# Kernel optimization log

Measured on AMD Instinct MI355X. Metric: run time of the kernel, lower is better.

The kernel has to match this reference:

```python
import jax, jax.numpy as jnp
import numpy as np

EPSILON = 0.1   # entropic regularization (reg)
TOL = 0.01      # stopThr
N_ITERS = 50    # numItermax
S_MASS = 0.9    # partial transported mass m (a,b normalized to sum 1 so s <= 1 is valid)
N, M = 2048, 2048


def _epot(C, a, b):
    """Faithful jax port of POT's entropic_partial_wasserstein with the EPOT
    module's marginal normalization. Fixed-point iteration with row-scaling,
    col-scaling, total-mass scaling and q1/q2/q3 correction matrices, with
    early-stop semantics (err checked every 10 iters) emulated via a done flag."""
    a = a / jnp.sum(a)
    b = b / jnp.sum(b)
    K0 = jnp.exp(-C / EPSILON)
    K0 = K0 * (S_MASS / jnp.sum(K0))
    ones = jnp.ones_like(K0)

    def body(carry, _):
        K, q1, q2, q3, err, cpt, done = carry
        Kprev = K
        # row scaling (clamped at 1 for partial mass)
        Kq = K * q1
        row = jnp.minimum(a / jnp.sum(Kq, axis=1), 1.0)          # (n,)
        K1 = row[:, None] * Kq
        q1n = q1 * Kprev / K1
        # col scaling
        K1prev = K1
        K1q = K1 * q2
        col = jnp.minimum(b / jnp.sum(K1q, axis=0), 1.0)         # (m,)
        K2 = K1q * col[None, :]
        q2n = q2 * K1prev / K2
        # total mass scaling
        K2prev = K2
        K2q = K2 * q3
        Kn = K2q * (S_MASS / jnp.sum(K2q))
        q3n = q3 * K2prev / Kn
        # POT updates err only every 10 iterations
        errn = jnp.where(cpt % 10 == 0,
                         jnp.sqrt(jnp.sum((Kprev - Kn) ** 2)), err)
        keep = lambda new, old: jnp.where(done, old, new)
        K = keep(Kn, K)
        q1 = keep(q1n, q1)
        q2 = keep(q2n, q2)
        q3 = keep(q3n, q3)
        err = jnp.where(done, err, errn)
        cpt = jnp.where(done, cpt, cpt + 1)
        done = done | (err <= TOL)
        return (K, q1, q2, q3, err, cpt, done), None

    init = (K0, ones, ones, ones, jnp.float32(1.0), jnp.int32(0),
            jnp.array(False))
    (K, _, _, _, _, _, _), _ = jax.lax.scan(body, init, None, length=N_ITERS)
    return K


def setup_inputs() -> dict:
    key = jax.random.key(0)
    k1, k2, k3 = jax.random.split(key, 3)
    C = jax.random.uniform(k1, (N, M), dtype=jnp.float32)
    a = jax.random.uniform(k2, (N,), dtype=jnp.float32) + 0.1
    b = jax.random.uniform(k3, (M,), dtype=jnp.float32) + 0.1
    return {"C": C, "a": a, "b": b}


def reference(C, a, b):
    return _epot(C, a, b)
```

## Files before the change

kernel.cpp:

```cpp
#include <hip/hip_runtime.h>

static constexpr int    N      = 2048;
static constexpr int    NBLK   = 256;
static constexpr int    NTHR   = 1024;
static constexpr int    RPB    = 8;
static constexpr double D_MASS = 0.9;
static constexpr double D_TOL  = 0.01;
static constexpr int    NITER  = 50;

struct Ws {
    double a_sum, b_sum;
    double bandSum[NBLK];
    double rowSum[N];
    double dotParts[NBLK];
    double errParts[NBLK];
    float  U[N], V[N];
    double Ud[N], rpD[N], Vd[N], cpD[N], UpD[N], VpD[N];
    float  partialT[(size_t)N * NBLK];
};

__device__ __forceinline__ double block_reduce(double v, double* s16) {
    for (int off = 32; off; off >>= 1) v += __shfl_xor(v, off, 64);
    const int wave = threadIdx.x >> 6, lane = threadIdx.x & 63;
    __syncthreads();
    if (lane == 0) s16[wave] = v;
    __syncthreads();
    double s = 0.0;
    #pragma unroll
    for (int w = 0; w < 16; ++w) s += s16[w];
    return s;
}

__global__ void __launch_bounds__(NTHR)
k1_sums(const float* __restrict__ C, const float* __restrict__ a,
        const float* __restrict__ b, Ws* __restrict__ ws)
{
    __shared__ double s16[16];
    const int tid = threadIdx.x, bid = blockIdx.x, lane = tid & 63;
    const int r0 = bid * RPB, rloc = tid >> 7, cgrp = tid & 127;

    if (bid == 0) {
        double t = block_reduce((double)a[tid] + (double)a[tid + 1024], s16);
        if (tid == 0) ws->a_sum = t;
    } else if (bid == 1) {
        double t = block_reduce((double)b[tid] + (double)b[tid + 1024], s16);
        if (tid == 0) ws->b_sum = t;
    }

    const int i = r0 + rloc;
    const float4* c4 = (const float4*)(C + (size_t)i * N);
    double s = 0.0;
    #pragma unroll 4
    for (int j4 = cgrp; j4 < N / 4; j4 += 128) {
        float4 c = c4[j4];
        s += (double)expf(-10.0f * c.x) + (double)expf(-10.0f * c.y)
           + (double)expf(-10.0f * c.z) + (double)expf(-10.0f * c.w);
    }
    for (int off = 32; off; off >>= 1) s += __shfl_xor(s, off, 64);
    __syncthreads();
    if (lane == 0) s16[tid >> 6] = s;
    __syncthreads();
    if (tid < RPB) ws->rowSum[r0 + tid] = s16[2 * tid] + s16[2 * tid + 1];
    if (tid == 0) {
        double bs = 0.0;
        #pragma unroll
        for (int w = 0; w < 16; ++w) bs += s16[w];
        ws->bandSum[bid] = bs;
    }
}

__global__ void __launch_bounds__(NTHR)
k2_rowscale_colpart(const float* __restrict__ C, const float* __restrict__ a,
                    Ws* __restrict__ ws)
{
    __shared__ double s16[16];
    __shared__ double sU[RPB];
    const int tid = threadIdx.x, bid = blockIdx.x;
    const int r0 = bid * RPB;

    const double k0sum = block_reduce((tid < NBLK) ? ws->bandSum[tid] : 0.0, s16);
    const double W0 = D_MASS / k0sum;

    if (tid < RPB) {
        const int i = r0 + tid;
        double r = ((double)a[i] / ws->a_sum) / (W0 * ws->rowSum[i]);
        if (r > 1.0) r = 1.0;
        sU[tid] = r;
        ws->U[i] = (float)r;
    }
    __syncthreads();

    double ub[RPB];
    #pragma unroll
    for (int r = 0; r < RPB; ++r) ub[r] = sU[r];
    const int j0 = 2 * tid;
    double ax = 0.0, ay = 0.0;
    #pragma unroll
    for (int r = 0; r < RPB; ++r) {
        const float2 c = *(const float2*)(C + (size_t)(r0 + r) * N + j0);
        ax += (double)expf(-10.0f * c.x) * ub[r];
        ay += (double)expf(-10.0f * c.y) * ub[r];
    }
    ws->partialT[(size_t)j0 * NBLK + bid]       = (float)ax;
    ws->partialT[(size_t)(j0 + 1) * NBLK + bid] = (float)ay;
}

__global__ void __launch_bounds__(256)
k3_colscale(const float* __restrict__ b, Ws* __restrict__ ws)
{
    __shared__ double s4[4];
    __shared__ double sT[RPB], sD[RPB];
    const int tid = threadIdx.x, bid = blockIdx.x;

    double v = (double)ws->bandSum[tid];
    for (int off = 32; off; off >>= 1) v += __shfl_xor(v, off, 64);
    if ((tid & 63) == 0) s4[tid >> 6] = v;
    __syncthreads();
    const double W0 = D_MASS / (s4[0] + s4[1] + s4[2] + s4[3]);

    const int jj = tid >> 5, p = tid & 31;
    const int j = bid * RPB + jj;
    double t = 0.0;
    #pragma unroll
    for (int q = 0; q < 8; ++q)
        t += (double)ws->partialT[(size_t)j * NBLK + p + 32 * q];
    for (int off = 16; off; off >>= 1) t += __shfl_xor(t, off, 64);
    if (p == 0) sT[jj] = t;
    __syncthreads();

    if (tid < RPB) {
        const int jc = bid * RPB + tid;
        const double Tj = sT[tid];
        double cf = ((double)b[jc] / ws->b_sum) / (W0 * Tj);
        if (cf > 1.0) cf = 1.0;
        ws->V[jc] = (float)cf;
        sD[tid] = Tj * cf;
    }
    __syncthreads();
    if (tid == 0) {
        double d = 0.0;
        #pragma unroll
        for (int q = 0; q < RPB; ++q) d += sD[q];
        ws->dotParts[bid] = d;
    }
}

__global__ void __launch_bounds__(NTHR)
k4_err_out(const float* __restrict__ C, float* __restrict__ K, Ws* __restrict__ ws)
{
    __shared__ double s16[16];
    const int tid = threadIdx.x, bid = blockIdx.x;
    const int r0 = bid * RPB, rloc = tid >> 7, cgrp = tid & 127;

    const double sd = block_reduce((tid < NBLK) ? ws->dotParts[tid] : 0.0, s16);
    const double Wn = D_MASS / sd;
    const double k0sum = block_reduce((tid < NBLK) ? ws->bandSum[tid] : 0.0, s16);
    const double upw = D_MASS / k0sum;

    const int i = r0 + rloc;
    const double unw = Wn * (double)ws->U[i];
    const float4* c4  = (const float4*)(C + (size_t)i * N);
    const float4* vn4 = (const float4*)ws->V;
    float4* k4p = (float4*)(K + (size_t)i * N);
    double e2 = 0.0;
    #pragma unroll 4
    for (int j4 = cgrp; j4 < N / 4; j4 += 128) {
        float4 c = c4[j4], vn = vn4[j4];
        const double k0x = (double)expf(-10.0f * c.x);
        const double k0y = (double)expf(-10.0f * c.y);
        const double k0z = (double)expf(-10.0f * c.z);
        const double k0w = (double)expf(-10.0f * c.w);
        float4 kn;
        kn.x = (float)(unw * k0x * (double)vn.x);
        kn.y = (float)(unw * k0y * (double)vn.y);
        kn.z = (float)(unw * k0z * (double)vn.z);
        kn.w = (float)(unw * k0w * (double)vn.w);
        k4p[j4] = kn;
        double d;
        d = k0x * (upw - unw * (double)vn.x); e2 += d * d;
        d = k0y * (upw - unw * (double)vn.y); e2 += d * d;
        d = k0z * (upw - unw * (double)vn.z); e2 += d * d;
        d = k0w * (upw - unw * (double)vn.w); e2 += d * d;
    }
    const double be = block_reduce(e2, s16);
    if (tid == 0) ws->errParts[bid] = be;
}

__global__ void __launch_bounds__(NTHR)
k5_decide_fallback(const float* __restrict__ C, const float* __restrict__ a,
                   const float* __restrict__ b, float* __restrict__ K,
                   Ws* __restrict__ ws)
{
    __shared__ double s16[16];
    const int tid = threadIdx.x;

    const double te0 = block_reduce((tid < NBLK) ? ws->errParts[tid] : 0.0, s16);
    if (sqrt(te0) <= D_TOL) return;

    const double a_sum = ws->a_sum, b_sum = ws->b_sum;
    const double sd0 = block_reduce((tid < NBLK) ? ws->dotParts[tid] : 0.0, s16);
    double W = D_MASS / sd0;

    for (int i = tid; i < N; i += NTHR) {
        ws->Ud[i]  = (double)ws->U[i];
        ws->rpD[i] = ws->Ud[i];
        ws->Vd[i]  = (double)ws->V[i];
        ws->cpD[i] = ws->Vd[i];
        ws->UpD[i] = 1.0; ws->VpD[i] = 1.0;
    }
    __syncthreads();

    double Wp = 0.0;
    bool done = false;
    for (int cpt = 1; cpt < NITER && !done; ++cpt) {
        const bool erriter = (cpt % 10) == 0;
        if (erriter) {
            Wp = W;
            for (int i = tid; i < N; i += NTHR) {
                ws->UpD[i] = ws->Ud[i]; ws->VpD[i] = ws->Vd[i];
            }
        }
        __syncthreads();

        for (int i = tid; i < N; i += NTHR) {
            const float* crow = C + (size_t)i * N;
            double s = 0.0;
            for (int j = 0; j < N; ++j)
                s += (double)expf(-10.0f * crow[j]) * ws->Vd[j];
            const double Uq = ws->Ud[i] / ws->rpD[i];
            double r = ((double)a[i] / a_sum) / (Uq * W * s);
            if (r > 1.0) r = 1.0;
            ws->Ud[i] = Uq * r; ws->rpD[i] = r;
        }
        __syncthreads();

        double dloc = 0.0;
        for (int j = tid; j < N; j += NTHR) {
            double t = 0.0;
            for (int i = 0; i < N; ++i)
                t += (double)expf(-10.0f * C[(size_t)i * N + j]) * ws->Ud[i];
            const double Vq = ws->Vd[j] / ws->cpD[j];
            double cf = ((double)b[j] / b_sum) / (Vq * W * t);
            if (cf > 1.0) cf = 1.0;
            const double Vn = Vq * cf;
            ws->Vd[j] = Vn; ws->cpD[j] = cf;
            dloc += t * Vn;
        }
        const double sd = block_reduce(dloc, s16);
        W = D_MASS / sd;

        if (erriter) {
            double e2 = 0.0;
            for (int i = tid; i < N; i += NTHR) {
                const float* crow = C + (size_t)i * N;
                const double up = Wp * ws->UpD[i];
                const double un = W  * ws->Ud[i];
                for (int j = 0; j < N; ++j) {
                    const double k0 = (double)expf(-10.0f * crow[j]);
                    const double d = k0 * (up * ws->VpD[j] - un * ws->Vd[j]);
                    e2 += d * d;
                }
            }
            const double te = block_reduce(e2, s16);
            done = (sqrt(te) <= D_TOL);
        }
        __syncthreads();
    }

    for (int i = tid; i < N; i += NTHR) {
        const float* crow = C + (size_t)i * N;
        float* krow = K + (size_t)i * N;
        const double uw = W * ws->Ud[i];
        for (int j = 0; j < N; ++j)
            krow[j] = (float)(uw * (double)expf(-10.0f * crow[j]) * ws->Vd[j]);
    }
}

extern "C" void kernel_launch(void* const* d_in, const int* in_sizes, int n_in,
                              void* d_out, int out_size, void* d_ws, size_t ws_size,
                              hipStream_t stream) {
    const float* C = (const float*)d_in[0];
    const float* a = (const float*)d_in[1];
    const float* b = (const float*)d_in[2];
    float* K = (float*)d_out;
    Ws*    w = (Ws*)d_ws;

    k1_sums<<<NBLK, NTHR, 0, stream>>>(C, a, b, w);
    k2_rowscale_colpart<<<NBLK, NTHR, 0, stream>>>(C, a, w);
    k3_colscale<<<NBLK, 256, 0, stream>>>(b, w);
    k4_err_out<<<NBLK, NTHR, 0, stream>>>(C, K, w);
    k5_decide_fallback<<<1, NTHR, 0, stream>>>(C, a, b, K, w);
}
```

Baseline: 33.67 us.

## Expand first-iteration error algebraically and fuse decision into output kernel

Computes the first-iteration Frobenius error from precomputed moment sums (sum K0^2, sum K0^2*u*v, sum K0^2*u^2*v^2) gathered during the earlier passes, so the output kernel no longer computes a per-element error. The convergence check and fallback now live in the output kernel, which drops the separate single-block decision kernel launch. The cost is two extra float partial-sum arrays written in k2 and read in k3. The expanded-square formula may lose precision through cancellation, and all blocks except block 0 exit early on the fallback path.

```diff
diff --git a/kernel.cpp b/kernel.cpp
--- a/kernel.cpp
+++ b/kernel.cpp
@@ -11,12 +11,14 @@
 struct Ws {
     double a_sum, b_sum;
     double bandSum[NBLK];
+    double s2Band[NBLK];
     double rowSum[N];
-    double dotParts[NBLK];
-    double errParts[NBLK];
+    double dotParts[NBLK], errAParts[NBLK], errBParts[NBLK];
     float  U[N], V[N];
     double Ud[N], rpD[N], Vd[N], cpD[N], UpD[N], VpD[N];
     float  partialT[(size_t)N * NBLK];
+    float  partialG[(size_t)N * NBLK];
+    float  partialH[(size_t)N * NBLK];
 };
 
 __device__ __forceinline__ double block_reduce(double v, double* s16) {
@@ -49,12 +51,16 @@
 
     const int i = r0 + rloc;
     const float4* c4 = (const float4*)(C + (size_t)i * N);
-    double s = 0.0;
+    double s = 0.0, s2 = 0.0;
     #pragma unroll 4
     for (int j4 = cgrp; j4 < N / 4; j4 += 128) {
         float4 c = c4[j4];
-        s += (double)expf(-10.0f * c.x) + (double)expf(-10.0f * c.y)
-           + (double)expf(-10.0f * c.z) + (double)expf(-10.0f * c.w);
+        const double ex = (double)expf(-10.0f * c.x);
+        const double ey = (double)expf(-10.0f * c.y);
+        const double ez = (double)expf(-10.0f * c.z);
+        const double ew = (double)expf(-10.0f * c.w);
+        s  += ex + ey + ez + ew;
+        s2 += ex * ex + ey * ey + ez * ez + ew * ew;
     }
     for (int off = 32; off; off >>= 1) s += __shfl_xor(s, off, 64);
     __syncthreads();
@@ -67,6 +73,8 @@
         for (int w = 0; w < 16; ++w) bs += s16[w];
         ws->bandSum[bid] = bs;
     }
+    const double bs2 = block_reduce(s2, s16);
+    if (tid == 0) ws->s2Band[bid] = bs2;
 }
 
 __global__ void __launch_bounds__(NTHR)
@@ -90,26 +98,34 @@
     }
     __syncthreads();
 
-    double ub[RPB];
-    #pragma unroll
-    for (int r = 0; r < RPB; ++r) ub[r] = sU[r];
+    double ub[RPB], ub2[RPB];
+    #pragma unroll
+    for (int r = 0; r < RPB; ++r) { ub[r] = sU[r]; ub2[r] = sU[r] * sU[r]; }
     const int j0 = 2 * tid;
-    double ax = 0.0, ay = 0.0;
+    double ax = 0.0, ay = 0.0, gx = 0.0, gy = 0.0, hx = 0.0, hy = 0.0;
     #pragma unroll
     for (int r = 0; r < RPB; ++r) {
         const float2 c = *(const float2*)(C + (size_t)(r0 + r) * N + j0);
-        ax += (double)expf(-10.0f * c.x) * ub[r];
-        ay += (double)expf(-10.0f * c.y) * ub[r];
+        const double ex = (double)expf(-10.0f * c.x);
+        const double ey = (double)expf(-10.0f * c.y);
+        ax += ex * ub[r];            ay += ey * ub[r];
+        gx += ex * ex * ub[r];       gy += ey * ey * ub[r];
+        hx += ex * ex * ub2[r];      hy += ey * ey * ub2[r];
     }
     ws->partialT[(size_t)j0 * NBLK + bid]       = (float)ax;
     ws->partialT[(size_t)(j0 + 1) * NBLK + bid] = (float)ay;
+    ws->partialG[(size_t)j0 * NBLK + bid]       = (float)gx;
+    ws->partialG[(size_t)(j0 + 1) * NBLK + bid] = (float)gy;
+    ws->partialH[(size_t)j0 * NBLK + bid]       = (float)hx;
+    ws->partialH[(size_t)(j0 + 1) * NBLK + bid] = (float)hy;
 }
 
 __global__ void __launch_bounds__(256)
 k3_colscale(const float* __restrict__ b, Ws* __restrict__ ws)
 {
     __shared__ double s4[4];
-    __shared__ double sT[RPB], sD[RPB];
+    __shared__ double sT[RPB], sG[RPB], sH[RPB];
+    __shared__ double sD[RPB], sA[RPB], sB[RPB];
     const int tid = threadIdx.x, bid = blockIdx.x;
 
     double v = (double)ws->bandSum[tid];
@@ -120,12 +136,21 @@
 
     const int jj = tid >> 5, p = tid & 31;
     const int j = bid * RPB + jj;
-    double t = 0.0;
-    #pragma unroll
-    for (int q = 0; q < 8; ++q)
-        t += (double)ws->partialT[(size_t)j * NBLK + p + 32 * q];
-    for (int off = 16; off; off >>= 1) t += __shfl_xor(t, off, 64);
-    if (p == 0) sT[jj] = t;
+    double t = 0.0, g = 0.0, h = 0.0;
+    #pragma unroll
+    for (int q = 0; q < 8; ++q) {
+        const size_t idx = (size_t)j * NBLK + p + 32 * q;
+        t += (double)ws->partialT[idx];
+        g += (double)ws->partialG[idx];
+        h += (double)ws->partialH[idx];
+    }
+    #pragma unroll
+    for (int off = 16; off; off >>= 1) {
+        t += __shfl_xor(t, off, 64);
+        g += __shfl_xor(g, off, 64);
+        h += __shfl_xor(h, off, 64);
+    }
+    if (p == 0) { sT[jj] = t; sG[jj] = g; sH[jj] = h; }
     __syncthreads();
 
     if (tid < RPB) {
@@ -135,71 +160,60 @@
         if (cf > 1.0) cf = 1.0;
         ws->V[jc] = (float)cf;
         sD[tid] = Tj * cf;
+        sA[tid] = sG[tid] * cf;
+        sB[tid] = sH[tid] * cf * cf;
     }
     __syncthreads();
     if (tid == 0) {
-        double d = 0.0;
+        double d = 0.0, ea = 0.0, eb = 0.0;
         #pragma unroll
-        for (int q = 0; q < RPB; ++q) d += sD[q];
+        for (int q = 0; q < RPB; ++q) { d += sD[q]; ea += sA[q]; eb += sB[q]; }
         ws->dotParts[bid] = d;
+        ws->errAParts[bid] = ea;
+        ws->errBParts[bid] = eb;
     }
 }
 
 __global__ void __launch_bounds__(NTHR)
-k4_err_out(const float* __restrict__ C, float* __restrict__ K, Ws* __restrict__ ws)
+k4_decide_out(const float* __restrict__ C, const float* __restrict__ a,
+              const float* __restrict__ b, float* __restrict__ K,
+              Ws* __restrict__ ws)
 {
     __shared__ double s16[16];
     const int tid = threadIdx.x, bid = blockIdx.x;
     const int r0 = bid * RPB, rloc = tid >> 7, cgrp = tid & 127;
 
-    const double sd = block_reduce((tid < NBLK) ? ws->dotParts[tid] : 0.0, s16);
+    const double sd    = block_reduce((tid < NBLK) ? ws->dotParts[tid]  : 0.0, s16);
+    const double errAs = block_reduce((tid < NBLK) ? ws->errAParts[tid] : 0.0, s16);
+    const double errBs = block_reduce((tid < NBLK) ? ws->errBParts[tid] : 0.0, s16);
+    const double s2tot = block_reduce((tid < NBLK) ? ws->s2Band[tid]    : 0.0, s16);
+    const double k0sum = block_reduce((tid < NBLK) ? ws->bandSum[tid]   : 0.0, s16);
+    const double W0 = D_MASS / k0sum;
     const double Wn = D_MASS / sd;
-    const double k0sum = block_reduce((tid < NBLK) ? ws->bandSum[tid] : 0.0, s16);
-    const double upw = D_MASS / k0sum;
-
-    const int i = r0 + rloc;
-    const double unw = Wn * (double)ws->U[i];
-    const float4* c4  = (const float4*)(C + (size_t)i * N);
-    const float4* vn4 = (const float4*)ws->V;
-    float4* k4p = (float4*)(K + (size_t)i * N);
-    double e2 = 0.0;
-    #pragma unroll 4
-    for (int j4 = cgrp; j4 < N / 4; j4 += 128) {
-        float4 c = c4[j4], vn = vn4[j4];
-        const double k0x = (double)expf(-10.0f * c.x);
-        const double k0y = (double)expf(-10.0f * c.y);
-        const double k0z = (double)expf(-10.0f * c.z);
-        const double k0w = (double)expf(-10.0f * c.w);
-        float4 kn;
-        kn.x = (float)(unw * k0x * (double)vn.x);
-        kn.y = (float)(unw * k0y * (double)vn.y);
-        kn.z = (float)(unw * k0z * (double)vn.z);
-        kn.w = (float)(unw * k0w * (double)vn.w);
-        k4p[j4] = kn;
-        double d;
-        d = k0x * (upw - unw * (double)vn.x); e2 += d * d;
-        d = k0y * (upw - unw * (double)vn.y); e2 += d * d;
-        d = k0z * (upw - unw * (double)vn.z); e2 += d * d;
-        d = k0w * (upw - unw * (double)vn.w); e2 += d * d;
-    }
-    const double be = block_reduce(e2, s16);
-    if (tid == 0) ws->errParts[bid] = be;
-}
-
-__global__ void __launch_bounds__(NTHR)
-k5_decide_fallback(const float* __restrict__ C, const float* __restrict__ a,
-                   const float* __restrict__ b, float* __restrict__ K,
-                   Ws* __restrict__ ws)
-{
-    __shared__ double s16[16];
-    const int tid = threadIdx.x;
-
-    const double te0 = block_reduce((tid < NBLK) ? ws->errParts[tid] : 0.0, s16);
-    if (sqrt(te0) <= D_TOL) return;
-
+    const double err2 = W0 * W0 * s2tot - 2.0 * W0 * Wn * errAs + Wn * Wn * errBs;
+
+    if (sqrt(err2) <= D_TOL) {
+        const int i = r0 + rloc;
+        const double unw = Wn * (double)ws->U[i];
+        const float4* c4  = (const float4*)(C + (size_t)i * N);
+        const float4* vn4 = (const float4*)ws->V;
+        float4* k4p = (float4*)(K + (size_t)i * N);
+        #pragma unroll 4
+        for (int j4 = cgrp; j4 < N / 4; j4 += 128) {
+            float4 c = c4[j4], vn = vn4[j4];
+            float4 kn;
+            kn.x = (float)(unw * (double)expf(-10.0f * c.x) * (double)vn.x);
+            kn.y = (float)(unw * (double)expf(-10.0f * c.y) * (double)vn.y);
+            kn.z = (float)(unw * (double)expf(-10.0f * c.z) * (double)vn.z);
+            kn.w = (float)(unw * (double)expf(-10.0f * c.w) * (double)vn.w);
+            k4p[j4] = kn;
+        }
+        return;
+    }
+
+    if (bid != 0) return;
     const double a_sum = ws->a_sum, b_sum = ws->b_sum;
-    const double sd0 = block_reduce((tid < NBLK) ? ws->dotParts[tid] : 0.0, s16);
-    double W = D_MASS / sd0;
+    double W = Wn;
 
     for (int i = tid; i < N; i += NTHR) {
         ws->Ud[i]  = (double)ws->U[i];
@@ -246,8 +260,8 @@
             ws->Vd[j] = Vn; ws->cpD[j] = cf;
             dloc += t * Vn;
         }
-        const double sd = block_reduce(dloc, s16);
-        W = D_MASS / sd;
+        const double sdl = block_reduce(dloc, s16);
+        W = D_MASS / sdl;
 
         if (erriter) {
             double e2 = 0.0;
@@ -288,6 +302,5 @@
     k1_sums<<<NBLK, NTHR, 0, stream>>>(C, a, b, w);
     k2_rowscale_colpart<<<NBLK, NTHR, 0, stream>>>(C, a, w);
     k3_colscale<<<NBLK, 256, 0, stream>>>(b, w);
-    k4_err_out<<<NBLK, NTHR, 0, stream>>>(C, K, w);
-    k5_decide_fallback<<<1, NTHR, 0, stream>>>(C, a, b, K, w);
-}
+    k4_decide_out<<<NBLK, NTHR, 0, stream>>>(C, a, b, K, w);
+}
```

Measured after the change: 49.08 us. 1.46x slower.

## Store column partials block-major and coalesce column reduction in k3

Applied to the files above, without the earlier changes.

The per-block column partial sums in k2 move from a column-major strided scatter to a block-major layout, written with contiguous float2 stores. k3 is rebuilt to match: 64 blocks of 1024 threads each cover 32 columns, read the partials coalesced, and reduce them through a padded shared-memory tile. This replaces the uncoalesced scattered writes and strided reads of the old layout. The dotParts array shrinks to 64 entries and its consumers are updated to sum over K3BLK.

```diff
diff --git a/kernel.cpp b/kernel.cpp
--- a/kernel.cpp
+++ b/kernel.cpp
@@ -4,6 +4,7 @@
 static constexpr int    NBLK   = 256;
 static constexpr int    NTHR   = 1024;
 static constexpr int    RPB    = 8;
+static constexpr int    K3BLK  = 64;
 static constexpr double D_MASS = 0.9;
 static constexpr double D_TOL  = 0.01;
 static constexpr int    NITER  = 50;
@@ -12,11 +13,11 @@
     double a_sum, b_sum;
     double bandSum[NBLK];
     double rowSum[N];
-    double dotParts[NBLK];
+    double dotParts[K3BLK];
     double errParts[NBLK];
     float  U[N], V[N];
     double Ud[N], rpD[N], Vd[N], cpD[N], UpD[N], VpD[N];
-    float  partialT[(size_t)N * NBLK];
+    float  partialT[(size_t)NBLK * N];
 };
 
 __device__ __forceinline__ double block_reduce(double v, double* s16) {
@@ -101,46 +102,45 @@
         ax += (double)expf(-10.0f * c.x) * ub[r];
         ay += (double)expf(-10.0f * c.y) * ub[r];
     }
-    ws->partialT[(size_t)j0 * NBLK + bid]       = (float)ax;
-    ws->partialT[(size_t)(j0 + 1) * NBLK + bid] = (float)ay;
-}
-
-__global__ void __launch_bounds__(256)
+    float2 o; o.x = (float)ax; o.y = (float)ay;
+    *(float2*)(ws->partialT + (size_t)bid * N + j0) = o;
+}
+
+__global__ void __launch_bounds__(NTHR)
 k3_colscale(const float* __restrict__ b, Ws* __restrict__ ws)
 {
-    __shared__ double s4[4];
-    __shared__ double sT[RPB], sD[RPB];
+    __shared__ double s16[16];
+    __shared__ double sAcc[32][33];
+    __shared__ double sD[32];
     const int tid = threadIdx.x, bid = blockIdx.x;
 
-    double v = (double)ws->bandSum[tid];
-    for (int off = 32; off; off >>= 1) v += __shfl_xor(v, off, 64);
-    if ((tid & 63) == 0) s4[tid >> 6] = v;
-    __syncthreads();
-    const double W0 = D_MASS / (s4[0] + s4[1] + s4[2] + s4[3]);
-
-    const int jj = tid >> 5, p = tid & 31;
-    const int j = bid * RPB + jj;
+    const double k0sum = block_reduce((tid < NBLK) ? ws->bandSum[tid] : 0.0, s16);
+    const double W0 = D_MASS / k0sum;
+
+    const int s = tid >> 5, c = tid & 31;
+    const int j = 32 * bid + c;
     double t = 0.0;
     #pragma unroll
     for (int q = 0; q < 8; ++q)
-        t += (double)ws->partialT[(size_t)j * NBLK + p + 32 * q];
-    for (int off = 16; off; off >>= 1) t += __shfl_xor(t, off, 64);
-    if (p == 0) sT[jj] = t;
-    __syncthreads();
-
-    if (tid < RPB) {
-        const int jc = bid * RPB + tid;
-        const double Tj = sT[tid];
-        double cf = ((double)b[jc] / ws->b_sum) / (W0 * Tj);
+        t += (double)ws->partialT[(size_t)(s + 32 * q) * N + j];
+    sAcc[s][c] = t;
+    __syncthreads();
+
+    if (tid < 32) {
+        double T = 0.0;
+        #pragma unroll
+        for (int q = 0; q < 32; ++q) T += sAcc[q][tid];
+        const int jc = 32 * bid + tid;
+        double cf = ((double)b[jc] / ws->b_sum) / (W0 * T);
         if (cf > 1.0) cf = 1.0;
         ws->V[jc] = (float)cf;
-        sD[tid] = Tj * cf;
+        sD[tid] = T * cf;
     }
     __syncthreads();
     if (tid == 0) {
         double d = 0.0;
         #pragma unroll
-        for (int q = 0; q < RPB; ++q) d += sD[q];
+        for (int q = 0; q < 32; ++q) d += sD[q];
         ws->dotParts[bid] = d;
     }
 }
@@ -152,7 +152,7 @@
     const int tid = threadIdx.x, bid = blockIdx.x;
     const int r0 = bid * RPB, rloc = tid >> 7, cgrp = tid & 127;
 
-    const double sd = block_reduce((tid < NBLK) ? ws->dotParts[tid] : 0.0, s16);
+    const double sd = block_reduce((tid < K3BLK) ? ws->dotParts[tid] : 0.0, s16);
     const double Wn = D_MASS / sd;
     const double k0sum = block_reduce((tid < NBLK) ? ws->bandSum[tid] : 0.0, s16);
     const double upw = D_MASS / k0sum;
@@ -198,7 +198,7 @@
     if (sqrt(te0) <= D_TOL) return;
 
     const double a_sum = ws->a_sum, b_sum = ws->b_sum;
-    const double sd0 = block_reduce((tid < NBLK) ? ws->dotParts[tid] : 0.0, s16);
+    const double sd0 = block_reduce((tid < K3BLK) ? ws->dotParts[tid] : 0.0, s16);
     double W = D_MASS / sd0;
 
     for (int i = tid; i < N; i += NTHR) {
@@ -287,7 +287,7 @@
 
     k1_sums<<<NBLK, NTHR, 0, stream>>>(C, a, b, w);
     k2_rowscale_colpart<<<NBLK, NTHR, 0, stream>>>(C, a, w);
-    k3_colscale<<<NBLK, 256, 0, stream>>>(b, w);
+    k3_colscale<<<K3BLK, NTHR, 0, stream>>>(b, w);
     k4_err_out<<<NBLK, NTHR, 0, stream>>>(C, K, w);
     k5_decide_fallback<<<1, NTHR, 0, stream>>>(C, a, b, K, w);
 }
```

Result: faster. 30.20 us (-10.3%).
